# Kernel tuning notes

Hardware: AMD Instinct MI355X
Metric: run time of the kernel (lower is better)

The kernel has to match this reference:

```python
import jax, jax.numpy as jnp
import numpy as np

MODEL_DIM = 1024
HEAD_SIZE = 128

def setup_inputs() -> dict:
    key = jax.random.key(0)
    k0, k1, k2, k3 = jax.random.split(key, 4)
    embedded = jax.random.normal(k0, (4, 4096, MODEL_DIM), dtype=jnp.float32)
    # nn.Linear(model_dim, head_size, bias=False) weights: [head_size, model_dim]
    s = 1.0 / np.sqrt(MODEL_DIM)
    Wk = jax.random.uniform(k1, (HEAD_SIZE, MODEL_DIM), jnp.float32, -s, s)
    Wq = jax.random.uniform(k2, (HEAD_SIZE, MODEL_DIM), jnp.float32, -s, s)
    Wv = jax.random.uniform(k3, (HEAD_SIZE, MODEL_DIM), jnp.float32, -s, s)
    return {"embedded": embedded, "Wk": Wk, "Wq": Wq, "Wv": Wv}

def reference(embedded, Wk, Wq, Wv):
    # embedded: [b, s, m]; W*: [h, m]
    keys = jnp.einsum('bsm,hm->bsh', embedded, Wk)
    queries = jnp.einsum('bsm,hm->bsh', embedded, Wq)
    values = jnp.einsum('bsm,hm->bsh', embedded, Wv)
    h = keys.shape[-1]
    scores = jnp.einsum('bqh,bkh->bqk', queries, keys) / jnp.sqrt(jnp.float32(h))  # [b,s,s]
    s_len = keys.shape[1]
    causal = jnp.tril(jnp.ones((s_len, s_len), dtype=bool))
    scores = jnp.where(causal, scores, -jnp.inf)
    probs = jax.nn.softmax(scores, axis=-1)
    return jnp.einsum('bqk,bkh->bqh', probs, values)
```

## Files before the change

### kernel.cpp

```cpp
#include <hip/hip_runtime.h>
#include <hip/hip_bf16.h>


#define SEQ 4096
#define BATCH 4
#define HS 128
#define SLOTS_PB 128

typedef unsigned short u16;
typedef __bf16 bf16x8 __attribute__((ext_vector_type(8)));
typedef _Float16 f16x4 __attribute__((ext_vector_type(4)));
typedef float f32x4 __attribute__((ext_vector_type(4)));

__device__ __forceinline__ u16 f2bf(float f) {
    union { float f; unsigned u; } v; v.f = f;
    unsigned u = v.u;
    return (u16)((u + 0x7FFFu + ((u >> 16) & 1u)) >> 16);
}
__device__ __forceinline__ float bf2f(u16 u) {
    union { unsigned u; float f; } v; v.u = ((unsigned)u) << 16; return v.f;
}
__device__ __forceinline__ u16 f2h(float f) {
    union { _Float16 h; u16 u; } v; v.h = (_Float16)f; return v.u;
}
__device__ __forceinline__ void async_cp16(const void* g, void* l) {
    __builtin_amdgcn_global_load_lds(
        (const __attribute__((address_space(1))) unsigned int*)g,
        (__attribute__((address_space(3))) unsigned int*)l, 16, 0, 0);
}
__device__ __forceinline__ int nsplit_of(int Q) {
    return Q / 5 + 1 + (Q >= 23 ? 1 : 0);
}

__global__ __launch_bounds__(256) void wconv_kernel(
    const float* __restrict__ Wk, const float* __restrict__ Wq,
    const float* __restrict__ Wv, u16* __restrict__ Wt)
{
    const int g    = blockIdx.x * 256 + threadIdx.x;
    const int lane = g & 63;
    const int kf   = (g >> 6) & 1;
    const int kc   = (g >> 7) & 15;
    const int nt   = g >> 11;
    const int row  = nt * 16 + (lane & 15);
    const int k0   = kc * 64 + kf * 32 + (lane >> 4) * 8;
    const float* src = (row < 128) ? Wk : ((row < 256) ? Wq : Wv);
    const float scale = (row >= 128 && row < 256)
        ? 0.08838834764831845f * 1.4426950408889634f : 1.0f;
    const float4 v0 = *(const float4*)&src[(size_t)(row & 127) * 1024 + k0];
    const float4 v1 = *(const float4*)&src[(size_t)(row & 127) * 1024 + k0 + 4];
    ushort4 a, b;
    a.x = f2bf(v0.x * scale); a.y = f2bf(v0.y * scale);
    a.z = f2bf(v0.z * scale); a.w = f2bf(v0.w * scale);
    b.x = f2bf(v1.x * scale); b.y = f2bf(v1.y * scale);
    b.z = f2bf(v1.z * scale); b.w = f2bf(v1.w * scale);
    *(ushort4*)&Wt[(size_t)g * 8]     = a;
    *(ushort4*)&Wt[(size_t)g * 8 + 4] = b;
}

__global__ __launch_bounds__(256, 2) void qkv_kernel(
    const float* __restrict__ emb, const u16* __restrict__ Wt,
    u16* __restrict__ Qf, u16* __restrict__ Kf, u16* __restrict__ Vf)
{
    __shared__ u16 sE[2][32][72];
    __shared__ u16 sOut[32][392];

    const int tid  = threadIdx.x;
    const int wv   = tid >> 6;
    const int lane = tid & 63;
    const int quad = lane >> 4;
    const int l16  = lane & 15;
    const int R0   = blockIdx.x * 32;

    const int arow = tid >> 3, ac8 = tid & 7;
    const float* abase = &emb[(size_t)(R0 + arow) * 1024 + ac8 * 8];

    f32x4 acc[2][6];
    #pragma unroll
    for (int rg = 0; rg < 2; rg++)
        #pragma unroll
        for (int nt = 0; nt < 6; nt++) acc[rg][nt] = (f32x4){0.f, 0.f, 0.f, 0.f};

    bf16x8 B0[12], B1[12];

#define LOADB(kci, B)                                                          \
    {                                                                          \
        _Pragma("unroll")                                                      \
        for (int nt = 0; nt < 6; nt++) {                                       \
            const size_t g = ((size_t)((wv * 6 + nt) * 16 + (kci)) * 2) * 64 + lane; \
            B[2 * nt]     = *(const bf16x8*)&Wt[g * 8];                        \
            B[2 * nt + 1] = *(const bf16x8*)&Wt[(g + 64) * 8];                 \
        }                                                                      \
    }
#define WRITEA(buf, v0, v1)                                                    \
    {                                                                          \
        ushort4 lo, hi;                                                        \
        lo.x = f2bf((v0).x); lo.y = f2bf((v0).y);                              \
        lo.z = f2bf((v0).z); lo.w = f2bf((v0).w);                              \
        hi.x = f2bf((v1).x); hi.y = f2bf((v1).y);                              \
        hi.z = f2bf((v1).z); hi.w = f2bf((v1).w);                              \
        *(ushort4*)&sE[buf][arow][ac8 * 8]     = lo;                           \
        *(ushort4*)&sE[buf][arow][ac8 * 8 + 4] = hi;                           \
    }
#define COMPUTE(buf, B)                                                        \
    {                                                                          \
        bf16x8 a[2][2];                                                        \
        _Pragma("unroll")                                                      \
        for (int rg = 0; rg < 2; rg++)                                         \
            _Pragma("unroll")                                                  \
            for (int kf = 0; kf < 2; kf++)                                     \
                a[rg][kf] = *(const bf16x8*)&sE[buf][rg * 16 + l16][kf * 32 + quad * 8]; \
        _Pragma("unroll")                                                      \
        for (int nt = 0; nt < 6; nt++)                                         \
            _Pragma("unroll")                                                  \
            for (int rg = 0; rg < 2; rg++) {                                   \
                acc[rg][nt] = __builtin_amdgcn_mfma_f32_16x16x32_bf16(a[rg][0], B[2 * nt],     acc[rg][nt], 0, 0, 0); \
                acc[rg][nt] = __builtin_amdgcn_mfma_f32_16x16x32_bf16(a[rg][1], B[2 * nt + 1], acc[rg][nt], 0, 0, 0); \
            }                                                                  \
    }

    float4 av0 = *(const float4*)&abase[0];
    float4 av1 = *(const float4*)&abase[4];
    LOADB(0, B0);
    WRITEA(0, av0, av1);

    for (int it = 0; it < 8; it++) {
        const int k1 = 2 * it + 1;
        __syncthreads();
        av0 = *(const float4*)&abase[k1 * 64];
        av1 = *(const float4*)&abase[k1 * 64 + 4];
        LOADB(k1, B1);
        COMPUTE(0, B0);
        WRITEA(1, av0, av1);
        __syncthreads();
        if (it < 7) {
            av0 = *(const float4*)&abase[(k1 + 1) * 64];
            av1 = *(const float4*)&abase[(k1 + 1) * 64 + 4];
            LOADB(k1 + 1, B0);
        }
        COMPUTE(1, B1);
        if (it < 7) WRITEA(0, av0, av1);
    }

    #pragma unroll
    for (int nt = 0; nt < 6; nt++) {
        const int col = wv * 96 + nt * 16 + l16;
        #pragma unroll
        for (int rg = 0; rg < 2; rg++) {
            const int rl = rg * 16 + quad * 4;
            #pragma unroll
            for (int r = 0; r < 4; r++) {
                const float v = acc[rg][nt][r];
                sOut[rl + r][col] = (col < 256) ? f2bf(v) : f2h(v);
            }
        }
    }
    __syncthreads();

    const int b  = R0 >> 12;
    const int s0 = R0 & 4095;
    #pragma unroll
    for (int i = 0; i < 2; i++) {
        const int g    = tid + i * 256;
        const int lg   = g & 63;
        const int kfp  = (g >> 6) & 3;
        const int k16l = g >> 8;
        const int rl   = k16l * 16 + (lg & 15);
        const int cl   = kfp * 32 + (lg >> 4) * 8;
        const size_t base = (((size_t)(b * 256 + (s0 >> 4) + k16l) * 4 + kfp) * 64 + lg) * 8;
        *(uint4*)&Kf[base] = *(const uint4*)&sOut[rl][cl];
        *(uint4*)&Qf[base] = *(const uint4*)&sOut[rl][128 + cl];
    }
    #pragma unroll
    for (int i = 0; i < 4; i++) {
        const int g   = tid + i * 256;
        const int lg  = g & 63;
        const int ntl = (g >> 6) & 1;
        const int ht  = g >> 7;
        const int h   = ht * 16 + (lg & 15);
        const int kl  = ntl * 16 + ((lg >> 4) & 3) * 4;
        ushort4 o;
        o.x = sOut[kl + 0][256 + h];
        o.y = sOut[kl + 1][256 + h];
        o.z = sOut[kl + 2][256 + h];
        o.w = sOut[kl + 3][256 + h];
        const int t64 = s0 >> 6;
        const int ntg = ((s0 >> 4) & 3) + ntl;
        const size_t base = ((((size_t)(b * 64 + t64) * 8 + ht) * 4 + ntg) * 64 + lg) * 4;
        *(ushort4*)&Vf[base] = o;
    }
#undef LOADB
#undef WRITEA
#undef COMPUTE
}

template<bool DIRECT>
__global__ __launch_bounds__(512, 4) void attn_kernel(
    const u16* __restrict__ Qf, const u16* __restrict__ Kf,
    const u16* __restrict__ Vf, u16* __restrict__ Opart,
    float* __restrict__ lpart, float* __restrict__ out)
{
    __shared__ u16 sT[2][16384];

    const int tid  = threadIdx.x;
    const int wv   = tid >> 6;
    const int lane = tid & 63;
    const int quad = lane >> 4;
    const int l16  = lane & 15;

    const int L    = blockIdx.x;
    const int b    = L & 3;
    const int slot = L >> 2;

    int Q = 0, sp = 0;
    if constexpr (DIRECT) {
        Q = slot; sp = 0;
    } else {
        int acc = 0;
        #pragma unroll 1
        for (int qq = 0; qq < 32; ++qq) {
            const int n = nsplit_of(qq);
            if (slot < acc + n) { Q = qq; sp = slot - acc; break; }
            acc += n;
        }
    }
    const int total = 2 * Q + 2;
    const int ns    = DIRECT ? 1 : nsplit_of(Q);
    const int kbeg  = DIRECT ? 0 : (sp * total) / ns;
    const int kend  = DIRECT ? total : ((sp + 1) * total) / ns;

    const int q0 = Q * 128;
    const size_t bS = (size_t)b * SEQ;

    const char* KbB = (const char*)(Kf + (size_t)b * 524288);
    const char* VbB = (const char*)(Vf + (size_t)b * 524288);

    bf16x8 qf[4];
    const int q16 = Q * 8 + wv;
    #pragma unroll
    for (int kf = 0; kf < 4; kf++)
        qf[kf] = *(const bf16x8*)&Qf[(((size_t)(b * 256 + q16) * 4 + kf) * 64 + lane) * 8];

    float rs0 = 0.f;
    f32x4 O[8];
    #pragma unroll
    for (int ht = 0; ht < 8; ht++) O[ht] = (f32x4){0.f, 0.f, 0.f, 0.f};

    const int qg0 = q0 + wv * 16 + l16;

    const int lseg = wv * 1024 + lane * 16;
#define STAGE(bufi, kt)                                                        \
    {                                                                          \
        const char* ks = KbB + (size_t)(kt) * 16384;                           \
        const char* vs = VbB + (size_t)(kt) * 16384;                           \
        char* lb = (char*)&sT[bufi][0] + wv * 1024;                            \
        _Pragma("unroll")                                                      \
        for (int i = 0; i < 2; i++)                                            \
            async_cp16(ks + i * 8192 + lseg, lb + i * 8192);                   \
        _Pragma("unroll")                                                      \
        for (int i = 0; i < 2; i++)                                            \
            async_cp16(vs + i * 8192 + lseg, lb + 16384 + i * 8192);           \
    }

    STAGE(0, kbeg);
    __syncthreads();

    int buf = 0;
    for (int kt = kbeg; kt < kend; ++kt) {
        const int kb = kt * 64;
        if (kt + 1 < kend) STAGE(buf ^ 1, kt + 1);

        const bool diag = (kt >= 2 * Q);
        f16x4 pf0[4];
        #pragma unroll
        for (int nt = 0; nt < 4; nt++) {
            f32x4 s0 = (f32x4){0.f, 0.f, 0.f, 0.f};
            #pragma unroll
            for (int kf = 0; kf < 4; kf++) {
                const bf16x8 kfr = *(const bf16x8*)&sT[buf][((nt * 4 + kf) << 9) + lane * 8];
                s0 = __builtin_amdgcn_mfma_f32_16x16x32_bf16(kfr, qf[kf], s0, 0, 0, 0);
            }
            if (diag) {
                #pragma unroll
                for (int r = 0; r < 4; r++) {
                    const int kg = kb + nt * 16 + quad * 4 + r;
                    if (kg > qg0) s0[r] = -3.0e38f;
                }
            }
            f16x4 p0;
            #pragma unroll
            for (int r = 0; r < 4; r++) {
                const float e0 = exp2f(s0[r] - 4.0f);
                rs0 += e0;
                p0[r] = (_Float16)e0;
            }
            pf0[nt] = p0;
        }

        #pragma unroll
        for (int ht = 0; ht < 8; ht++) {
            f16x4 vf[4];
            #pragma unroll
            for (int nt = 0; nt < 4; nt++)
                vf[nt] = *(const f16x4*)&sT[buf][8192 + ((ht * 4 + nt) << 8) + lane * 4];
            #pragma unroll
            for (int nt = 0; nt < 4; nt++)
                O[ht] = __builtin_amdgcn_mfma_f32_16x16x16f16(vf[nt], pf0[nt], O[ht], 0, 0, 0);
        }

        __syncthreads();
        buf ^= 1;
    }
#undef STAGE

    rs0 += __shfl_xor(rs0, 16); rs0 += __shfl_xor(rs0, 32);

    if constexpr (DIRECT) {
        const float inv = 1.0f / rs0;
        const int q = q0 + wv * 16 + l16;
        #pragma unroll
        for (int ht = 0; ht < 8; ht++) {
            f32x4 o = O[ht] * inv;
            *(f32x4*)&out[(bS + q) * HS + ht * 16 + quad * 4] = o;
        }
    } else {
        const size_t slotbase = (size_t)b * SLOTS_PB + slot;
        #pragma unroll
        for (int ht = 0; ht < 8; ht++) {
            const size_t j = ((slotbase * 8 + wv) * 8 + ht) * 64 + lane;
            ushort4 o;
            o.x = f2bf(O[ht][0]); o.y = f2bf(O[ht][1]);
            o.z = f2bf(O[ht][2]); o.w = f2bf(O[ht][3]);
            *(ushort4*)&Opart[j * 4] = o;
        }
        if (quad == 0)
            lpart[slotbase * 128 + wv * 16 + l16] = rs0;
    }
}

__global__ __launch_bounds__(256) void merge_kernel(
    const u16* __restrict__ Opart, const float* __restrict__ lpart,
    float* __restrict__ out)
{
    const int g  = blockIdx.x * 256 + threadIdx.x;
    const int b  = g >> 17;
    const int q  = (g >> 5) & 4095;
    const int hc = g & 31;
    const int Q  = q >> 7;
    const int ql = q & 127;
    const int wvv = ql >> 4, l16 = q & 15;
    const int ht = hc >> 2, qd = hc & 3;
    const int lane = qd * 16 + l16;

    int pre = 0, ns = 0;
    #pragma unroll 1
    for (int qq = 0; qq < 32; ++qq) {
        const int n = nsplit_of(qq);
        if (qq < Q) pre += n;
        else if (qq == Q) { ns = n; break; }
    }
    const size_t base_slot = (size_t)b * SLOTS_PB + pre;

    float den = 0.f;
    f32x4 num = (f32x4){0.f, 0.f, 0.f, 0.f};
    #pragma unroll 1
    for (int s = 0; s < ns; s++) {
        den += lpart[(base_slot + s) * 128 + ql];
        const size_t j = (((base_slot + s) * 8 + wvv) * 8 + ht) * 64 + lane;
        const ushort4 o = *(const ushort4*)&Opart[j * 4];
        num[0] += bf2f(o.x); num[1] += bf2f(o.y);
        num[2] += bf2f(o.z); num[3] += bf2f(o.w);
    }
    const float inv = 1.0f / den;
    float4 o; o.x = num[0] * inv; o.y = num[1] * inv;
    o.z = num[2] * inv; o.w = num[3] * inv;
    *(float4*)&out[(size_t)g * 4] = o;
}

extern "C" void kernel_launch(void* const* d_in, const int* in_sizes, int n_in,
                              void* d_out, int out_size, void* d_ws, size_t ws_size,
                              hipStream_t stream) {
    const float* emb = (const float*)d_in[0];
    const float* Wk  = (const float*)d_in[1];
    const float* Wq  = (const float*)d_in[2];
    const float* Wv  = (const float*)d_in[3];
    float* out = (float*)d_out;

    char* ws = (char*)d_ws;
    const size_t WBF_SZ    = (size_t)384 * 1024 * 2;
    const size_t QKV_SZ    = (size_t)BATCH * SEQ * HS * 2;
    const size_t Q_OFF     = WBF_SZ;
    const size_t K_OFF     = Q_OFF + QKV_SZ;
    const size_t V_OFF     = K_OFF + QKV_SZ;
    const size_t OPART_OFF = V_OFF + QKV_SZ;
    const size_t OPART_SZ  = (size_t)BATCH * SLOTS_PB * 32768;
    const size_t L_SZ      = (size_t)BATCH * SLOTS_PB * 128 * 4;

    u16* Wt = (u16*)ws;
    u16* Qf = (u16*)(ws + Q_OFF);
    u16* Kf = (u16*)(ws + K_OFF);
    u16* Vf = (u16*)(ws + V_OFF);

    wconv_kernel<<<dim3(192), dim3(256), 0, stream>>>(Wk, Wq, Wv, Wt);
    qkv_kernel<<<dim3(512), dim3(256), 0, stream>>>(emb, Wt, Qf, Kf, Vf);

    const size_t need = OPART_OFF + OPART_SZ + L_SZ;

    if (ws_size >= need) {
        u16*   Opart = (u16*)(ws + OPART_OFF);
        float* lp    = (float*)(ws + OPART_OFF + OPART_SZ);
        attn_kernel<false><<<dim3(4 * SLOTS_PB), dim3(512), 0, stream>>>(Qf, Kf, Vf, Opart, lp, out);
        merge_kernel<<<dim3(BATCH * SEQ * HS / 4 / 256), dim3(256), 0, stream>>>(Opart, lp, out);
    } else {
        attn_kernel<true><<<dim3(32 * BATCH), dim3(512), 0, stream>>>(Qf, Kf, Vf, nullptr, nullptr, out);
    }
}
```

Before: 159.2 us.

## Restructure QKV projection into 64-row tiles with async LDS-staged weights; add MFMA priority hints

The QKV projection kernel now runs 256 blocks of 512 threads, each computing a 64-row tile. Weight fragments are staged into shared memory with async 16-byte copies instead of being loaded into registers per wave, and the K chunk drops to 32 so the buffers fit in a union with the output staging area. Eight waves now share each staged weight tile, which cuts global weight traffic and register pressure but doubles the barrier count per K pass. Separately, the attention kernel wraps its MFMA sections in s_setprio hints so matrix work is scheduled ahead of other waves.

```diff
diff --git a/kernel.cpp b/kernel.cpp
--- a/kernel.cpp
+++ b/kernel.cpp
@@ -57,100 +57,103 @@
     *(ushort4*)&Wt[(size_t)g * 8 + 4] = b;
 }
 
-__global__ __launch_bounds__(256, 2) void qkv_kernel(
+__global__ __launch_bounds__(512, 2) void qkv_kernel(
     const float* __restrict__ emb, const u16* __restrict__ Wt,
     u16* __restrict__ Qf, u16* __restrict__ Kf, u16* __restrict__ Vf)
 {
-    __shared__ u16 sE[2][32][72];
-    __shared__ u16 sOut[32][392];
+    __shared__ union {
+        struct {
+            u16 E[2][64][40];
+            u16 B[2][24][512];
+        } s;
+        u16 sOut[64][392];
+    } sm;
 
     const int tid  = threadIdx.x;
     const int wv   = tid >> 6;
     const int lane = tid & 63;
     const int quad = lane >> 4;
     const int l16  = lane & 15;
-    const int R0   = blockIdx.x * 32;
-
-    const int arow = tid >> 3, ac8 = tid & 7;
-    const float* abase = &emb[(size_t)(R0 + arow) * 1024 + ac8 * 8];
+    const int rg2  = wv >> 2;
+    const int cg   = wv & 3;
+    const int R0   = blockIdx.x * 64;
+
+    const int arow = tid >> 3, ak = tid & 7;
+    const float* abase = &emb[(size_t)(R0 + arow) * 1024 + ak * 4];
+    const char* WtB = (const char*)Wt;
 
     f32x4 acc[2][6];
     #pragma unroll
     for (int rg = 0; rg < 2; rg++)
         #pragma unroll
-        for (int nt = 0; nt < 6; nt++) acc[rg][nt] = (f32x4){0.f, 0.f, 0.f, 0.f};
-
-    bf16x8 B0[12], B1[12];
-
-#define LOADB(kci, B)                                                          \
+        for (int j = 0; j < 6; j++) acc[rg][j] = (f32x4){0.f, 0.f, 0.f, 0.f};
+
+#define LOADA(c) (*(const float4*)&abase[(size_t)(c) * 32])
+#define WRITEA(bufi, v)                                                        \
+    {                                                                          \
+        ushort4 o;                                                             \
+        o.x = f2bf((v).x); o.y = f2bf((v).y);                                  \
+        o.z = f2bf((v).z); o.w = f2bf((v).w);                                  \
+        *(ushort4*)&sm.s.E[bufi][arow][ak * 4] = o;                            \
+    }
+#define STAGEB(bufi, c)                                                        \
     {                                                                          \
         _Pragma("unroll")                                                      \
-        for (int nt = 0; nt < 6; nt++) {                                       \
-            const size_t g = ((size_t)((wv * 6 + nt) * 16 + (kci)) * 2) * 64 + lane; \
-            B[2 * nt]     = *(const bf16x8*)&Wt[g * 8];                        \
-            B[2 * nt + 1] = *(const bf16x8*)&Wt[(g + 64) * 8];                 \
+        for (int i = 0; i < 3; i++) {                                          \
+            const int nt = wv * 3 + i;                                         \
+            async_cp16(WtB + (size_t)(nt * 32 + (c)) * 1024 + lane * 16,       \
+                       (void*)&sm.s.B[bufi][nt][0]);                           \
         }                                                                      \
     }
-#define WRITEA(buf, v0, v1)                                                    \
+#define COMPUTE(bufi)                                                          \
     {                                                                          \
-        ushort4 lo, hi;                                                        \
-        lo.x = f2bf((v0).x); lo.y = f2bf((v0).y);                              \
-        lo.z = f2bf((v0).z); lo.w = f2bf((v0).w);                              \
-        hi.x = f2bf((v1).x); hi.y = f2bf((v1).y);                              \
-        hi.z = f2bf((v1).z); hi.w = f2bf((v1).w);                              \
-        *(ushort4*)&sE[buf][arow][ac8 * 8]     = lo;                           \
-        *(ushort4*)&sE[buf][arow][ac8 * 8 + 4] = hi;                           \
-    }
-#define COMPUTE(buf, B)                                                        \
-    {                                                                          \
-        bf16x8 a[2][2];                                                        \
+        bf16x8 a[2];                                                           \
         _Pragma("unroll")                                                      \
         for (int rg = 0; rg < 2; rg++)                                         \
+            a[rg] = *(const bf16x8*)&sm.s.E[bufi][rg2 * 32 + rg * 16 + l16][quad * 8]; \
+        _Pragma("unroll")                                                      \
+        for (int j = 0; j < 6; j++) {                                          \
+            const bf16x8 bfr = *(const bf16x8*)&sm.s.B[bufi][cg * 6 + j][lane * 8]; \
             _Pragma("unroll")                                                  \
-            for (int kf = 0; kf < 2; kf++)                                     \
-                a[rg][kf] = *(const bf16x8*)&sE[buf][rg * 16 + l16][kf * 32 + quad * 8]; \
-        _Pragma("unroll")                                                      \
-        for (int nt = 0; nt < 6; nt++)                                         \
-            _Pragma("unroll")                                                  \
-            for (int rg = 0; rg < 2; rg++) {                                   \
-                acc[rg][nt] = __builtin_amdgcn_mfma_f32_16x16x32_bf16(a[rg][0], B[2 * nt],     acc[rg][nt], 0, 0, 0); \
-                acc[rg][nt] = __builtin_amdgcn_mfma_f32_16x16x32_bf16(a[rg][1], B[2 * nt + 1], acc[rg][nt], 0, 0, 0); \
-            }                                                                  \
-    }
-
-    float4 av0 = *(const float4*)&abase[0];
-    float4 av1 = *(const float4*)&abase[4];
-    LOADB(0, B0);
-    WRITEA(0, av0, av1);
-
-    for (int it = 0; it < 8; it++) {
-        const int k1 = 2 * it + 1;
+            for (int rg = 0; rg < 2; rg++)                                     \
+                acc[rg][j] = __builtin_amdgcn_mfma_f32_16x16x32_bf16(a[rg], bfr, acc[rg][j], 0, 0, 0); \
+        }                                                                      \
+    }
+#define ITER(bufi, c)                                                          \
+    {                                                                          \
+        if ((c) < 31) STAGEB((bufi) ^ 1, (c) + 1);                             \
+        float4 avn{};                                                          \
+        if ((c) < 30) avn = LOADA((c) + 2);                                    \
+        COMPUTE(bufi);                                                         \
+        if ((c) < 31) WRITEA((bufi) ^ 1, av1);                                 \
+        av1 = avn;                                                             \
+        __syncthreads();                                                       \
+    }
+
+    float4 av1;
+    {
+        const float4 av0 = LOADA(0);
+        av1 = LOADA(1);
+        STAGEB(0, 0);
+        WRITEA(0, av0);
         __syncthreads();
-        av0 = *(const float4*)&abase[k1 * 64];
-        av1 = *(const float4*)&abase[k1 * 64 + 4];
-        LOADB(k1, B1);
-        COMPUTE(0, B0);
-        WRITEA(1, av0, av1);
-        __syncthreads();
-        if (it < 7) {
-            av0 = *(const float4*)&abase[(k1 + 1) * 64];
-            av1 = *(const float4*)&abase[(k1 + 1) * 64 + 4];
-            LOADB(k1 + 1, B0);
-        }
-        COMPUTE(1, B1);
-        if (it < 7) WRITEA(0, av0, av1);
+    }
+
+    for (int cc = 0; cc < 16; cc++) {
+        ITER(0, 2 * cc);
+        ITER(1, 2 * cc + 1);
     }
 
     #pragma unroll
     for (int nt = 0; nt < 6; nt++) {
-        const int col = wv * 96 + nt * 16 + l16;
+        const int col = cg * 96 + nt * 16 + l16;
         #pragma unroll
         for (int rg = 0; rg < 2; rg++) {
-            const int rl = rg * 16 + quad * 4;
+            const int rl = rg2 * 32 + rg * 16 + quad * 4;
             #pragma unroll
             for (int r = 0; r < 4; r++) {
                 const float v = acc[rg][nt][r];
-                sOut[rl + r][col] = (col < 256) ? f2bf(v) : f2h(v);
+                sm.sOut[rl + r][col] = (col < 256) ? f2bf(v) : f2h(v);
             }
         }
     }
@@ -160,37 +163,38 @@
     const int s0 = R0 & 4095;
     #pragma unroll
     for (int i = 0; i < 2; i++) {
-        const int g    = tid + i * 256;
+        const int g    = tid + i * 512;
         const int lg   = g & 63;
         const int kfp  = (g >> 6) & 3;
-        const int k16l = g >> 8;
+        const int k16l = (g >> 8) & 3;
         const int rl   = k16l * 16 + (lg & 15);
         const int cl   = kfp * 32 + (lg >> 4) * 8;
         const size_t base = (((size_t)(b * 256 + (s0 >> 4) + k16l) * 4 + kfp) * 64 + lg) * 8;
-        *(uint4*)&Kf[base] = *(const uint4*)&sOut[rl][cl];
-        *(uint4*)&Qf[base] = *(const uint4*)&sOut[rl][128 + cl];
+        *(uint4*)&Kf[base] = *(const uint4*)&sm.sOut[rl][cl];
+        *(uint4*)&Qf[base] = *(const uint4*)&sm.sOut[rl][128 + cl];
     }
     #pragma unroll
     for (int i = 0; i < 4; i++) {
-        const int g   = tid + i * 256;
+        const int g   = tid + i * 512;
         const int lg  = g & 63;
-        const int ntl = (g >> 6) & 1;
-        const int ht  = g >> 7;
+        const int ntl = (g >> 6) & 3;
+        const int ht  = g >> 8;
         const int h   = ht * 16 + (lg & 15);
         const int kl  = ntl * 16 + ((lg >> 4) & 3) * 4;
         ushort4 o;
-        o.x = sOut[kl + 0][256 + h];
-        o.y = sOut[kl + 1][256 + h];
-        o.z = sOut[kl + 2][256 + h];
-        o.w = sOut[kl + 3][256 + h];
+        o.x = sm.sOut[kl + 0][256 + h];
+        o.y = sm.sOut[kl + 1][256 + h];
+        o.z = sm.sOut[kl + 2][256 + h];
+        o.w = sm.sOut[kl + 3][256 + h];
         const int t64 = s0 >> 6;
-        const int ntg = ((s0 >> 4) & 3) + ntl;
-        const size_t base = ((((size_t)(b * 64 + t64) * 8 + ht) * 4 + ntg) * 64 + lg) * 4;
+        const size_t base = ((((size_t)(b * 64 + t64) * 8 + ht) * 4 + ntl) * 64 + lg) * 4;
         *(ushort4*)&Vf[base] = o;
     }
-#undef LOADB
+#undef LOADA
 #undef WRITEA
+#undef STAGEB
 #undef COMPUTE
+#undef ITER
 }
 
 template<bool DIRECT>
@@ -274,11 +278,13 @@
         #pragma unroll
         for (int nt = 0; nt < 4; nt++) {
             f32x4 s0 = (f32x4){0.f, 0.f, 0.f, 0.f};
+            __builtin_amdgcn_s_setprio(1);
             #pragma unroll
             for (int kf = 0; kf < 4; kf++) {
                 const bf16x8 kfr = *(const bf16x8*)&sT[buf][((nt * 4 + kf) << 9) + lane * 8];
                 s0 = __builtin_amdgcn_mfma_f32_16x16x32_bf16(kfr, qf[kf], s0, 0, 0, 0);
             }
+            __builtin_amdgcn_s_setprio(0);
             if (diag) {
                 #pragma unroll
                 for (int r = 0; r < 4; r++) {
@@ -296,6 +302,7 @@
             pf0[nt] = p0;
         }
 
+        __builtin_amdgcn_s_setprio(1);
         #pragma unroll
         for (int ht = 0; ht < 8; ht++) {
             f16x4 vf[4];
@@ -306,6 +313,7 @@
             for (int nt = 0; nt < 4; nt++)
                 O[ht] = __builtin_amdgcn_mfma_f32_16x16x16f16(vf[nt], pf0[nt], O[ht], 0, 0, 0);
         }
+        __builtin_amdgcn_s_setprio(0);
 
         __syncthreads();
         buf ^= 1;
@@ -401,7 +409,7 @@
     u16* Vf = (u16*)(ws + V_OFF);
 
     wconv_kernel<<<dim3(192), dim3(256), 0, stream>>>(Wk, Wq, Wv, Wt);
-    qkv_kernel<<<dim3(512), dim3(256), 0, stream>>>(emb, Wt, Qf, Kf, Vf);
+    qkv_kernel<<<dim3(256), dim3(512), 0, stream>>>(emb, Wt, Qf, Kf, Vf);
 
     const size_t need = OPART_OFF + OPART_SZ + L_SZ;
 
```

Measured after the change: 165.6 us. 4.0% more time.
